# Kernel optimization log

Measured on AMD Instinct MI355X. Metric: run time of the kernel, lower is better.

Reference implementation:

```python
import jax, jax.numpy as jnp
import numpy as np

B, NP, D, K, H = 2, 512, 768, 64, 8
HD = D // H  # head dim = 96


def layernorm(x, g, b, eps=1e-5):
    m = jnp.mean(x, axis=-1, keepdims=True)
    v = jnp.mean((x - m) ** 2, axis=-1, keepdims=True)
    return (x - m) / jnp.sqrt(v + eps) * g + b


def setup_inputs() -> dict:
    key = jax.random.key(0)
    ks = jax.random.split(key, 16)
    s = 0.02
    return {
        "features": jax.random.normal(ks[0], (B, NP, D), jnp.float32),
        "points_xyz": jax.random.normal(ks[1], (B, NP, 3), jnp.float32),
        # distance_encoder: Linear(1 -> D)
        "Wd": jax.random.normal(ks[2], (D,), jnp.float32) * s,
        "bd": jnp.zeros((D,), jnp.float32),
        # geo_attention: MultiheadAttention(D, H)
        "Wq": jax.random.normal(ks[3], (D, D), jnp.float32) * s,
        "bq": jnp.zeros((D,), jnp.float32),
        "Wk": jax.random.normal(ks[4], (D, D), jnp.float32) * s,
        "bk": jnp.zeros((D,), jnp.float32),
        "Wv": jax.random.normal(ks[5], (D, D), jnp.float32) * s,
        "bv": jnp.zeros((D,), jnp.float32),
        "Wo": jax.random.normal(ks[6], (D, D), jnp.float32) * s,
        "bo": jnp.zeros((D,), jnp.float32),
        # spatial_enhancer: Linear(2D -> D) + LayerNorm + SiLU
        "We": jax.random.normal(ks[7], (2 * D, D), jnp.float32) * s,
        "be": jnp.zeros((D,), jnp.float32),
        "g_ln": jnp.ones((D,), jnp.float32),
        "b_ln": jnp.zeros((D,), jnp.float32),
    }


def reference(features, points_xyz, Wd, bd, Wq, bq, Wk, bk, Wv, bv, Wo, bo, We, be, g_ln, b_ln):
    # pairwise distances per batch: [B, Np, Np]
    sq = jnp.sum(points_xyz ** 2, axis=-1)
    d2 = sq[:, :, None] + sq[:, None, :] - 2.0 * jnp.einsum("bnd,bmd->bnm", points_xyz, points_xyz)
    dist = jnp.sqrt(jnp.maximum(d2, 0.0))
    # k nearest neighbors (smallest distances)
    neg_d, idx = jax.lax.top_k(-dist, K)          # idx: [B, Np, K]
    nbr_dist = -neg_d                              # [B, Np, K]
    # gather neighbor features: [B, Np, K, D]
    nbr_feat = jax.vmap(lambda f, i: f[i])(features, idx)
    # distance encoder: Linear(1->D) on unsqueezed distances
    dist_feat = nbr_dist[..., None] * Wd + bd      # [B, Np, K, D]
    kv = nbr_feat + dist_feat
    # multi-head attention: per-point query over its K neighbors
    q = (features @ Wq + bq).reshape(B, NP, H, HD)
    k = (kv @ Wk + bk).reshape(B, NP, K, H, HD)
    v = (kv @ Wv + bv).reshape(B, NP, K, H, HD)
    scores = jnp.einsum("bnhd,bnkhd->bnhk", q, k) / jnp.sqrt(jnp.float32(HD))
    attn = jax.nn.softmax(scores, axis=-1)
    o = jnp.einsum("bnhk,bnkhd->bnhd", attn, v).reshape(B, NP, D)
    attended = o @ Wo + bo                          # [B, Np, D]
    # spatial enhancer on [features ; attended]
    ctx = jnp.concatenate([features, attended], axis=-1)
    enhanced = jax.nn.silu(layernorm(ctx @ We + be, g_ln, b_ln))
    return enhanced
```

## Files before the change

### kernel.cpp

```cpp
#include <hip/hip_runtime.h>
#include <math.h>

#define NPTS 512
#define DIM  768
#define KNN  64
#define NH   8
#define HDIM 96
#define MROWS 1024
#define MPAD  1088
#define WOROWS 832
#define WSQ   ((size_t)DIM * DIM)

typedef unsigned short u16;
typedef unsigned long long ull;
typedef __attribute__((ext_vector_type(8))) short short8;
typedef __attribute__((ext_vector_type(4))) float f32x4;

__device__ __forceinline__ unsigned f2bf(float f) {
    unsigned u = __float_as_uint(f);
    return (u + 0x7fffu + ((u >> 16) & 1u)) >> 16;
}
__device__ __forceinline__ float bf2f(u16 v) {
    return __uint_as_float(((unsigned)v) << 16);
}

__global__ __launch_bounds__(256) void mega_prep_k(
    const float* __restrict__ features,
    const float* __restrict__ Wd, const float* __restrict__ bd,
    const float* __restrict__ Wq, const float* __restrict__ Wk, const float* __restrict__ Wv,
    const float* __restrict__ Wo, const float* __restrict__ bo, const float* __restrict__ We,
    u16* __restrict__ Fb, u16* __restrict__ Wob, u16* __restrict__ W3)
{
    __shared__ float T[64][65];
    int bid = blockIdx.x, tid = threadIdx.x;

    if (bid < 768) {
        int i = (bid * 256 + tid) * 4;
        float4 v = *(const float4*)&features[i];
        uint2 o;
        o.x = f2bf(v.x) | (f2bf(v.y) << 16);
        o.y = f2bf(v.z) | (f2bf(v.w) << 16);
        *(uint2*)&Fb[i] = o;
        return;
    }
    if (bid < 816) {
        int flat = (bid - 768) * 1024 + tid * 4;
        int r = flat / DIM, c = flat - r * DIM;
        uint2 o; o.x = 0u; o.y = 0u;
        if (r == 0) {
            float4 v = *(const float4*)&Wd[c];
            o.x = f2bf(v.x) | (f2bf(v.y) << 16);
            o.y = f2bf(v.z) | (f2bf(v.w) << 16);
        } else if (r == 1) {
            float4 v = *(const float4*)&bd[c];
            o.x = f2bf(v.x) | (f2bf(v.y) << 16);
            o.y = f2bf(v.z) | (f2bf(v.w) << 16);
        }
        *(uint2*)&Fb[(size_t)(MROWS + r) * DIM + c] = o;
        return;
    }
    if (bid < 1440) {
        int flat = (bid - 816) * 1024 + tid * 4;
        int r = flat / DIM, c = flat - r * DIM;
        uint2 o; o.x = 0u; o.y = 0u;
        if (r < DIM) {
            float4 v = *(const float4*)&Wo[(size_t)r * DIM + c];
            o.x = f2bf(v.x) | (f2bf(v.y) << 16);
            o.y = f2bf(v.z) | (f2bf(v.w) << 16);
        } else if (r == DIM) {
            float4 v = *(const float4*)&bo[c];
            o.x = f2bf(v.x) | (f2bf(v.y) << 16);
            o.y = f2bf(v.z) | (f2bf(v.w) << 16);
        }
        *(uint2*)&Wob[(size_t)r * DIM + c] = o;
        return;
    }
    {
        int t = bid - 1440;
        int m = t / 144, r2 = t % 144;
        int by = r2 / 12, bx = r2 % 12;
        const float* S = (m == 0) ? Wq : (m == 1) ? Wk : (m == 2) ? Wv
                       : (m == 3) ? We : (We + WSQ);
        u16* D = W3 + (size_t)m * WSQ;
        int r0 = by * 64, c0 = bx * 64;
#pragma unroll
        for (int i = 0; i < 16; ++i) {
            int lin = tid + i * 256;
            int r = lin >> 6, c = lin & 63;
            T[r][c] = S[(size_t)(r0 + r) * DIM + c0 + c];
        }
        __syncthreads();
#pragma unroll
        for (int i = 0; i < 16; ++i) {
            int lin = tid + i * 256;
            int c = lin >> 6, r = lin & 63;
            D[(size_t)(c0 + c) * DIM + r0 + r] = (u16)f2bf(T[r][c]);
        }
    }
}

union alignas(16) GTSm {
    struct { short As[64][72]; short Bs[64][72]; } g;
    float P[NPTS * 3];
};

__global__ __launch_bounds__(256) void qkvw_topk_k(
    const u16* __restrict__ Fb, const u16* __restrict__ Wob, const u16* __restrict__ W3,
    const float* __restrict__ bq, const float* __restrict__ be,
    const float* __restrict__ pts,
    float* __restrict__ FQ, u16* __restrict__ FKb, u16* __restrict__ FVb,
    u16* __restrict__ WeffT, float* __restrict__ c_e, float* __restrict__ Z0,
    int* __restrict__ idxb, float* __restrict__ distb)
{
    __shared__ GTSm sm;
    int bid = blockIdx.x, tid = threadIdx.x;

    if (bid < 256) {
        int w = tid >> 6, lane = tid & 63;
        int bn = bid * 4 + w;
        int b  = bn >> 9;
        int n  = bn & (NPTS - 1);
        const float* pb = pts + (size_t)b * NPTS * 3;
        for (int i = tid; i < NPTS * 3; i += 256) sm.P[i] = pb[i];
        __syncthreads();

        float xn = sm.P[n * 3], yn = sm.P[n * 3 + 1], zn = sm.P[n * 3 + 2];
        float sqn = xn * xn + yn * yn + zn * zn;
        ull key[8];
#pragma unroll
        for (int r = 0; r < 8; ++r) {
            int m = r * 64 + lane;
            float xm = sm.P[m * 3], ym = sm.P[m * 3 + 1], zm = sm.P[m * 3 + 2];
            float d2 = sqn + (xm * xm + ym * ym + zm * zm)
                     - 2.0f * (xn * xm + yn * ym + zn * zm);
            unsigned db = __float_as_uint(fmaxf(d2, 0.0f));
            key[r] = ((ull)db << 32) | (unsigned)m;
        }

#pragma unroll
        for (int k = 2; k <= 512; k <<= 1) {
#pragma unroll
            for (int j = k >> 1; j > 0; j >>= 1) {
                if (j >= 64) {
                    int jr = j >> 6;
#pragma unroll
                    for (int r = 0; r < 8; ++r) {
                        if ((r & jr) == 0) {
                            int rp = r | jr;
                            bool up = (((r << 6) & k) == 0);
                            ull a = key[r], bk = key[rp];
                            bool alt = a < bk;
                            ull lo = alt ? a : bk, hi = alt ? bk : a;
                            key[r]  = up ? lo : hi;
                            key[rp] = up ? hi : lo;
                        }
                    }
                } else {
#pragma unroll
                    for (int r = 0; r < 8; ++r) {
                        unsigned lo32 = (unsigned)key[r];
                        unsigned hi32 = (unsigned)(key[r] >> 32);
                        unsigned plo = __shfl_xor(lo32, j);
                        unsigned phi = __shfl_xor(hi32, j);
                        ull p = ((ull)phi << 32) | plo;
                        bool keep_lo = ((((r << 6) | lane) & k) == 0) == ((lane & j) == 0);
                        bool alt = key[r] < p;
                        ull lo = alt ? key[r] : p, hi = alt ? p : key[r];
                        key[r] = keep_lo ? lo : hi;
                    }
                }
            }
        }

        ull k0 = key[0];
        idxb[(size_t)bn * KNN + lane]  = (int)(k0 & 0xffffffffu);
        distb[(size_t)bn * KNN + lane] = sqrtf(__uint_as_float((unsigned)(k0 >> 32)));
        return;
    }

    int bid2 = bid - 256;
    int z, by, bx;
    if (bid2 < 816) {
        z = bid2 / 204;
        int rem = bid2 - z * 204;
        by = rem / 12; bx = rem - by * 12;
        if (z == 0 && by >= 16) return;
        if (z == 3 && by >= 13) return;
    } else {
        z = 4;
        int rem = bid2 - 816;
        by = rem / 12; bx = rem - by * 12;
    }
    const u16* A  = (z == 3) ? Wob : Fb;
    const u16* BT = W3 + (size_t)((z == 3) ? 4 : (z == 4) ? 3 : z) * WSQ;

    int wave = tid >> 6, lane = tid & 63;
    int wr = (wave >> 1) * 32, wc = (wave & 1) * 32;
    int l15 = lane & 15, kg = lane >> 4;
    int brow = by * 64, bcol = bx * 64;

    f32x4 acc[2][2] = {};

    int srow = tid >> 3;
    int scol = (tid & 7) * 8;

    for (int k0 = 0; k0 < DIM; k0 += 64) {
#pragma unroll
        for (int s = 0; s < 2; ++s) {
            int r = srow + s * 32;
            *(short8*)&sm.g.As[r][scol] = *(const short8*)&A[(size_t)(brow + r) * DIM + k0 + scol];
            *(short8*)&sm.g.Bs[r][scol] = *(const short8*)&BT[(size_t)(bcol + r) * DIM + k0 + scol];
        }
        __syncthreads();
#pragma unroll
        for (int kk = 0; kk < 2; ++kk) {
            short8 a0 = *(const short8*)&sm.g.As[wr + l15][kk * 32 + kg * 8];
            short8 a1 = *(const short8*)&sm.g.As[wr + 16 + l15][kk * 32 + kg * 8];
            short8 b0 = *(const short8*)&sm.g.Bs[wc + l15][kk * 32 + kg * 8];
            short8 b1 = *(const short8*)&sm.g.Bs[wc + 16 + l15][kk * 32 + kg * 8];
            acc[0][0] = __builtin_amdgcn_mfma_f32_16x16x32_bf16(a0, b0, acc[0][0], 0, 0, 0);
            acc[0][1] = __builtin_amdgcn_mfma_f32_16x16x32_bf16(a0, b1, acc[0][1], 0, 0, 0);
            acc[1][0] = __builtin_amdgcn_mfma_f32_16x16x32_bf16(a1, b0, acc[1][0], 0, 0, 0);
            acc[1][1] = __builtin_amdgcn_mfma_f32_16x16x32_bf16(a1, b1, acc[1][1], 0, 0, 0);
        }
        __syncthreads();
    }

#pragma unroll
    for (int m = 0; m < 2; ++m) {
#pragma unroll
        for (int n = 0; n < 2; ++n) {
            int col  = bcol + wc + n * 16 + l15;
            int row0 = brow + wr + m * 16 + kg * 4;
            if (z == 0) {
                float bv = bq[col];
#pragma unroll
                for (int j = 0; j < 4; ++j)
                    FQ[(size_t)(row0 + j) * DIM + col] = acc[m][n][j] + bv;
            } else if (z == 1) {
#pragma unroll
                for (int j = 0; j < 4; ++j)
                    FKb[(size_t)(row0 + j) * DIM + col] = (u16)f2bf(acc[m][n][j]);
            } else if (z == 2) {
#pragma unroll
                for (int j = 0; j < 4; ++j)
                    FVb[(size_t)(row0 + j) * DIM + col] = (u16)f2bf(acc[m][n][j]);
            } else if (z == 4) {
                float bv = be[col];
#pragma unroll
                for (int j = 0; j < 4; ++j)
                    Z0[(size_t)(row0 + j) * DIM + col] = acc[m][n][j] + bv;
            } else {
                if (row0 + 3 < DIM) {
                    ull pk =
                          (ull)f2bf(acc[m][n][0])
                        | ((ull)f2bf(acc[m][n][1]) << 16)
                        | ((ull)f2bf(acc[m][n][2]) << 32)
                        | ((ull)f2bf(acc[m][n][3]) << 48);
                    *(ull*)&WeffT[(size_t)col * DIM + row0] = pk;
                } else {
#pragma unroll
                    for (int j = 0; j < 4; ++j) {
                        int row = row0 + j;
                        if (row < DIM)       WeffT[(size_t)col * DIM + row] = (u16)f2bf(acc[m][n][j]);
                        else if (row == DIM) c_e[col] = acc[m][n][j];
                    }
                }
            }
        }
    }
}

__global__ __launch_bounds__(256) void gemm_z1_k(
    const u16* __restrict__ Ob, const u16* __restrict__ WeffT,
    const float* __restrict__ c_e, float* __restrict__ Z1)
{
    __shared__ short As[64][72];
    __shared__ short Bs[64][72];

    int tid  = threadIdx.x;
    int wave = tid >> 6, lane = tid & 63;
    int wr = (wave >> 1) * 32, wc = (wave & 1) * 32;
    int l15 = lane & 15, kg = lane >> 4;
    int brow = blockIdx.y * 64, bcol = blockIdx.x * 64;

    f32x4 acc[2][2] = {};

    int srow = tid >> 3;
    int scol = (tid & 7) * 8;

    for (int k0 = 0; k0 < DIM; k0 += 64) {
#pragma unroll
        for (int s = 0; s < 2; ++s) {
            int r = srow + s * 32;
            *(short8*)&As[r][scol] = *(const short8*)&Ob[(size_t)(brow + r) * DIM + k0 + scol];
            *(short8*)&Bs[r][scol] = *(const short8*)&WeffT[(size_t)(bcol + r) * DIM + k0 + scol];
        }
        __syncthreads();
#pragma unroll
        for (int kk = 0; kk < 2; ++kk) {
            short8 a0 = *(const short8*)&As[wr + l15][kk * 32 + kg * 8];
            short8 a1 = *(const short8*)&As[wr + 16 + l15][kk * 32 + kg * 8];
            short8 b0 = *(const short8*)&Bs[wc + l15][kk * 32 + kg * 8];
            short8 b1 = *(const short8*)&Bs[wc + 16 + l15][kk * 32 + kg * 8];
            acc[0][0] = __builtin_amdgcn_mfma_f32_16x16x32_bf16(a0, b0, acc[0][0], 0, 0, 0);
            acc[0][1] = __builtin_amdgcn_mfma_f32_16x16x32_bf16(a0, b1, acc[0][1], 0, 0, 0);
            acc[1][0] = __builtin_amdgcn_mfma_f32_16x16x32_bf16(a1, b0, acc[1][0], 0, 0, 0);
            acc[1][1] = __builtin_amdgcn_mfma_f32_16x16x32_bf16(a1, b1, acc[1][1], 0, 0, 0);
        }
        __syncthreads();
    }

#pragma unroll
    for (int m = 0; m < 2; ++m) {
#pragma unroll
        for (int n = 0; n < 2; ++n) {
            int col = bcol + wc + n * 16 + l15;
            float bv = c_e[col];
#pragma unroll
            for (int j = 0; j < 4; ++j) {
                int row = brow + wr + m * 16 + kg * 4 + j;
                Z1[(size_t)row * DIM + col] = acc[m][n][j] + bv;
            }
        }
    }
}

__global__ __launch_bounds__(512) void attn_k(
    const float* __restrict__ FQ, const u16* __restrict__ FKb, const u16* __restrict__ FVb,
    const int* __restrict__ idxb, const float* __restrict__ distb,
    const float* __restrict__ bk, const float* __restrict__ bv,
    u16* __restrict__ O)
{
    int bn = blockIdx.x;
    int b  = bn >> 9;
    int tid = threadIdx.x;
    int wv = tid >> 6, lane = tid & 63;

    __shared__ float qlds[NH][104];
    __shared__ int   s_idx[KNN];
    __shared__ float s_dist[KNN];
    __shared__ float s_sc[NH][68];
    __shared__ float s_att[NH][68];
    __shared__ float s_qh[NH][2];
    __shared__ float s_sd[NH];

    if (tid < KNN) {
        s_idx[tid]  = idxb[(size_t)bn * KNN + tid];
        s_dist[tid] = distb[(size_t)bn * KNN + tid];
    }
    const float* qrow = FQ + (size_t)bn * DIM;
    {
        int d = tid;
        if (d < DIM) qlds[d / HDIM][d % HDIM] = qrow[d];
        int d2 = tid + 512;
        if (d2 < DIM) qlds[d2 / HDIM][d2 % HDIM] = qrow[d2];
    }
    __syncthreads();

    {
        int h = wv;
        const u16* wdk = FKb + (size_t)MROWS * DIM + h * HDIM;
        const u16* ckr = FKb + (size_t)(MROWS + 1) * DIM + h * HDIM;
        const float* bkh = bk + h * HDIM;
        float q = qlds[h][lane];
        float pw = q * bf2f(wdk[lane]);
        float pc = q * (bf2f(ckr[lane]) + bkh[lane]);
        if (lane < HDIM - 64) {
            float q2 = qlds[h][lane + 64];
            pw = fmaf(q2, bf2f(wdk[lane + 64]), pw);
            pc = fmaf(q2, bf2f(ckr[lane + 64]) + bkh[lane + 64], pc);
        }
#pragma unroll
        for (int off = 32; off; off >>= 1) {
            pw += __shfl_xor(pw, off);
            pc += __shfl_xor(pc, off);
        }
        if (lane == 0) { s_qh[h][0] = pw; s_qh[h][1] = pc; }
    }

    {
        int j = tid >> 3, h = tid & 7;
        const u16* kr = FKb + (size_t)(b * NPTS + s_idx[j]) * DIM + h * HDIM;
        const uint4* kr4 = (const uint4*)kr;
        float a0 = 0.f, a1 = 0.f, a2 = 0.f, a3 = 0.f;
#pragma unroll
        for (int i = 0; i < 12; ++i) {
            uint4 kv = kr4[i];
            float4 qa = *(const float4*)&qlds[h][i * 8];
            float4 qb = *(const float4*)&qlds[h][i * 8 + 4];
            a0 = fmaf(qa.x, __uint_as_float(kv.x << 16), a0);
            a1 = fmaf(qa.y, __uint_as_float(kv.x & 0xffff0000u), a1);
            a2 = fmaf(qa.z, __uint_as_float(kv.y << 16), a2);
            a3 = fmaf(qa.w, __uint_as_float(kv.y & 0xffff0000u), a3);
            a0 = fmaf(qb.x, __uint_as_float(kv.z << 16), a0);
            a1 = fmaf(qb.y, __uint_as_float(kv.z & 0xffff0000u), a1);
            a2 = fmaf(qb.z, __uint_as_float(kv.w << 16), a2);
            a3 = fmaf(qb.w, __uint_as_float(kv.w & 0xffff0000u), a3);
        }
        s_sc[h][j] = (a0 + a1) + (a2 + a3);
    }
    __syncthreads();

    {
        int h = wv, j = lane;
        const float invs = 0.10206207261596575f;
        float qwdk = s_qh[h][0], qck = s_qh[h][1];
        float dj = s_dist[j];
        float sc = (s_sc[h][j] + dj * qwdk + qck) * invs;
        float mx = sc;
#pragma unroll
        for (int off = 32; off; off >>= 1) mx = fmaxf(mx, __shfl_xor(mx, off));
        float ev = __expf(sc - mx);
        float sum = ev;
#pragma unroll
        for (int off = 32; off; off >>= 1) sum += __shfl_xor(sum, off);
        float att = ev / sum;
        s_att[h][j] = att;
        float sd = att * dj;
#pragma unroll
        for (int off = 32; off; off >>= 1) sd += __shfl_xor(sd, off);
        if (lane == 0) s_sd[h] = sd;
    }
    __syncthreads();

    if (tid < 384) {
        int d0 = tid * 2;
        int h  = d0 / HDIM;
        const float* attp = s_att[h];
        const size_t basev = (size_t)(b * NPTS) * DIM + d0;
        float o0 = 0.f, o1 = 0.f;
#pragma unroll 4
        for (int j = 0; j < KNN; ++j) {
            unsigned pv = *(const unsigned*)&FVb[basev + (size_t)s_idx[j] * DIM];
            float a = attp[j];
            o0 = fmaf(a, __uint_as_float(pv << 16), o0);
            o1 = fmaf(a, __uint_as_float(pv & 0xffff0000u), o1);
        }
        const u16* wdv = FVb + (size_t)MROWS * DIM;
        const u16* cvr = FVb + (size_t)(MROWS + 1) * DIM;
        float sdh = s_sd[h];
        o0 += sdh * bf2f(wdv[d0])     + (bf2f(cvr[d0])     + bv[d0]);
        o1 += sdh * bf2f(wdv[d0 + 1]) + (bf2f(cvr[d0 + 1]) + bv[d0 + 1]);
        unsigned po = f2bf(o0) | (f2bf(o1) << 16);
        *(unsigned*)&O[(size_t)bn * DIM + d0] = po;
    }
}

__global__ __launch_bounds__(192) void ln_silu_k(
    const float* __restrict__ Z0, const float* __restrict__ Z1,
    const float* __restrict__ g, const float* __restrict__ bta,
    float* __restrict__ out)
{
    int bn = blockIdx.x, tid = threadIdx.x;
    size_t ro = (size_t)bn * DIM;
    int e0 = tid * 4;
    float4 x = *(const float4*)&Z0[ro + e0];
    {
        float4 p = *(const float4*)&Z1[ro + e0];
        x.x += p.x; x.y += p.y; x.z += p.z; x.w += p.w;
    }
    float s  = (x.x + x.y) + (x.z + x.w);
    float ss = (x.x * x.x + x.y * x.y) + (x.z * x.z + x.w * x.w);
    __shared__ float red[3][2];
#pragma unroll
    for (int off = 32; off; off >>= 1) {
        s  += __shfl_xor(s, off);
        ss += __shfl_xor(ss, off);
    }
    int w = tid >> 6;
    if ((tid & 63) == 0) { red[w][0] = s; red[w][1] = ss; }
    __syncthreads();
    s  = red[0][0] + red[1][0] + red[2][0];
    ss = red[0][1] + red[1][1] + red[2][1];
    float mean = s * (1.0f / DIM);
    float var  = ss * (1.0f / DIM) - mean * mean;
    float rstd = rsqrtf(var + 1e-5f);
    float4 gv = *(const float4*)&g[e0];
    float4 bv = *(const float4*)&bta[e0];
    float4 y;
    y.x = (x.x - mean) * rstd * gv.x + bv.x;
    y.y = (x.y - mean) * rstd * gv.y + bv.y;
    y.z = (x.z - mean) * rstd * gv.z + bv.z;
    y.w = (x.w - mean) * rstd * gv.w + bv.w;
    float4 o;
    o.x = y.x / (1.0f + __expf(-y.x));
    o.y = y.y / (1.0f + __expf(-y.y));
    o.z = y.z / (1.0f + __expf(-y.z));
    o.w = y.w / (1.0f + __expf(-y.w));
    *(float4*)&out[ro + e0] = o;
}

extern "C" void kernel_launch(void* const* d_in, const int* in_sizes, int n_in,
                              void* d_out, int out_size, void* d_ws, size_t ws_size,
                              hipStream_t stream)
{
    const float* features = (const float*)d_in[0];
    const float* pts      = (const float*)d_in[1];
    const float* Wd       = (const float*)d_in[2];
    const float* bd       = (const float*)d_in[3];
    const float* Wq       = (const float*)d_in[4];
    const float* bq       = (const float*)d_in[5];
    const float* Wk       = (const float*)d_in[6];
    const float* bk       = (const float*)d_in[7];
    const float* Wv       = (const float*)d_in[8];
    const float* bv       = (const float*)d_in[9];
    const float* Wo       = (const float*)d_in[10];
    const float* bo       = (const float*)d_in[11];
    const float* We       = (const float*)d_in[12];
    const float* be       = (const float*)d_in[13];
    const float* g_ln     = (const float*)d_in[14];
    const float* b_ln     = (const float*)d_in[15];

    const size_t MAT  = (size_t)MROWS * DIM;
    const size_t MATP = (size_t)MPAD  * DIM;

    float* ws = (float*)d_ws;
    float* FQ    = ws;
    u16*   FKb   = (u16*)(ws + MATP);
    u16*   FVb   = FKb + MATP;
    u16*   Fb    = FVb + MATP;
    u16*   Ob    = Fb + MATP;
    u16*   Wob   = Ob + MAT;
    u16*   W3    = Wob + (size_t)WOROWS * DIM;
    u16*   WeffT = W3 + 5 * WSQ;
    float* c_e   = (float*)(WeffT + WSQ);
    int*   idxb  = (int*)(c_e + DIM);
    float* distb = (float*)(idxb + (size_t)MROWS * KNN);
    float* Z0    = distb + (size_t)MROWS * KNN;
    float* Z1    = Z0 + MAT;

    mega_prep_k<<<2160, 256, 0, stream>>>(features, Wd, bd, Wq, Wk, Wv, Wo, bo, We,
                                          Fb, Wob, W3);
    qkvw_topk_k<<<1264, 256, 0, stream>>>(
        Fb, Wob, W3, bq, be, pts, FQ, FKb, FVb, WeffT, c_e, Z0, idxb, distb);
    attn_k<<<MROWS, 512, 0, stream>>>(FQ, FKb, FVb, idxb, distb, bk, bv, Ob);
    gemm_z1_k<<<dim3(12, 16), 256, 0, stream>>>(Ob, WeffT, c_e, Z1);
    ln_silu_k<<<MROWS, 192, 0, stream>>>(Z0, Z1, g_ln, b_ln, (float*)d_out);
}
```

Measured before the change: 71.68 us.

## Use 128x128 GEMM tiles with direct global-to-LDS loads and XOR swizzle

Both bf16 GEMM paths (the fused QKV/weight-fold kernel and the Z1 GEMM) move from 64x64 to 128x128 block tiles, with each wave computing a 64x64 sub-tile of 4x4 MFMAs. Operand tiles are loaded with global_load_lds straight into shared memory, using an XOR-swizzled column layout in place of padded rows to avoid bank conflicts. Padding of the bf16 buffers is enlarged so the taller tiles stay in bounds. Block counts drop a lot (e.g. 48 blocks for the Z1 GEMM), which raises per-block reuse but lowers occupancy and parallelism on a GPU with many CUs.

New measurement: 77.17 us. +7.7%, slower.

```diff
diff --git a/kernel.cpp b/kernel.cpp
--- a/kernel.cpp
+++ b/kernel.cpp
@@ -7,8 +7,8 @@
 #define NH   8
 #define HDIM 96
 #define MROWS 1024
-#define MPAD  1088
-#define WOROWS 832
+#define MP2   1152
+#define WOR2  896
 #define WSQ   ((size_t)DIM * DIM)
 
 typedef unsigned short u16;
@@ -22,6 +22,11 @@
 }
 __device__ __forceinline__ float bf2f(u16 v) {
     return __uint_as_float(((unsigned)v) << 16);
+}
+__device__ __forceinline__ void gload_lds16(const void* g, void* l) {
+    __builtin_amdgcn_global_load_lds(
+        (const __attribute__((address_space(1))) void*)g,
+        (__attribute__((address_space(3))) void*)l, 16, 0, 0);
 }
 
 __global__ __launch_bounds__(256) void mega_prep_k(
@@ -43,7 +48,7 @@
         *(uint2*)&Fb[i] = o;
         return;
     }
-    if (bid < 816) {
+    if (bid < 864) {
         int flat = (bid - 768) * 1024 + tid * 4;
         int r = flat / DIM, c = flat - r * DIM;
         uint2 o; o.x = 0u; o.y = 0u;
@@ -59,8 +64,8 @@
         *(uint2*)&Fb[(size_t)(MROWS + r) * DIM + c] = o;
         return;
     }
-    if (bid < 1440) {
-        int flat = (bid - 816) * 1024 + tid * 4;
+    if (bid < 1536) {
+        int flat = (bid - 864) * 1024 + tid * 4;
         int r = flat / DIM, c = flat - r * DIM;
         uint2 o; o.x = 0u; o.y = 0u;
         if (r < DIM) {
@@ -76,7 +81,7 @@
         return;
     }
     {
-        int t = bid - 1440;
+        int t = bid - 1536;
         int m = t / 144, r2 = t % 144;
         int by = r2 / 12, bx = r2 % 12;
         const float* S = (m == 0) ? Wq : (m == 1) ? Wk : (m == 2) ? Wv
@@ -100,7 +105,7 @@
 }
 
 union alignas(16) GTSm {
-    struct { short As[64][72]; short Bs[64][72]; } g;
+    struct { short A[128 * 64]; short B[128 * 64]; } g;
     float P[NPTS * 3];
 };
 
@@ -114,10 +119,10 @@
 {
     __shared__ GTSm sm;
     int bid = blockIdx.x, tid = threadIdx.x;
+    int wv = tid >> 6, lane = tid & 63;
 
     if (bid < 256) {
-        int w = tid >> 6, lane = tid & 63;
-        int bn = bid * 4 + w;
+        int bn = bid * 4 + wv;
         int b  = bn >> 9;
         int n  = bn & (NPTS - 1);
         const float* pb = pts + (size_t)b * NPTS * 3;
@@ -180,58 +185,60 @@
 
     int bid2 = bid - 256;
     int z, by, bx;
-    if (bid2 < 816) {
-        z = bid2 / 204;
-        int rem = bid2 - z * 204;
-        by = rem / 12; bx = rem - by * 12;
-        if (z == 0 && by >= 16) return;
-        if (z == 3 && by >= 13) return;
-    } else {
-        z = 4;
-        int rem = bid2 - 816;
-        by = rem / 12; bx = rem - by * 12;
-    }
+    if (bid2 < 162)      { z = bid2 / 54; int r = bid2 % 54; by = r / 6; bx = r % 6; }
+    else if (bid2 < 204) { z = 3; int r = bid2 - 162; by = r / 6; bx = r % 6; }
+    else                 { z = 4; int r = bid2 - 204; by = r / 6; bx = r % 6; }
     const u16* A  = (z == 3) ? Wob : Fb;
     const u16* BT = W3 + (size_t)((z == 3) ? 4 : (z == 4) ? 3 : z) * WSQ;
 
-    int wave = tid >> 6, lane = tid & 63;
-    int wr = (wave >> 1) * 32, wc = (wave & 1) * 32;
+    int wr2 = (wv >> 1) * 64, wc2 = (wv & 1) * 64;
     int l15 = lane & 15, kg = lane >> 4;
-    int brow = by * 64, bcol = bx * 64;
-
-    f32x4 acc[2][2] = {};
-
-    int srow = tid >> 3;
-    int scol = (tid & 7) * 8;
+    int brow = by * 128, bcol = bx * 128;
+
+    f32x4 acc[4][4] = {};
 
     for (int k0 = 0; k0 < DIM; k0 += 64) {
 #pragma unroll
-        for (int s = 0; s < 2; ++s) {
-            int r = srow + s * 32;
-            *(short8*)&sm.g.As[r][scol] = *(const short8*)&A[(size_t)(brow + r) * DIM + k0 + scol];
-            *(short8*)&sm.g.Bs[r][scol] = *(const short8*)&BT[(size_t)(bcol + r) * DIM + k0 + scol];
+        for (int i = 0; i < 4; ++i) {
+            int flat = i * 256 + tid;
+            int row = flat >> 3, c = flat & 7;
+            int cs = c ^ (row & 7);
+            gload_lds16(&A[(size_t)(brow + row) * DIM + k0 + cs * 8],
+                        &sm.g.A[(i * 256 + wv * 64) * 8]);
+            gload_lds16(&BT[(size_t)(bcol + row) * DIM + k0 + cs * 8],
+                        &sm.g.B[(i * 256 + wv * 64) * 8]);
         }
         __syncthreads();
 #pragma unroll
         for (int kk = 0; kk < 2; ++kk) {
-            short8 a0 = *(const short8*)&sm.g.As[wr + l15][kk * 32 + kg * 8];
-            short8 a1 = *(const short8*)&sm.g.As[wr + 16 + l15][kk * 32 + kg * 8];
-            short8 b0 = *(const short8*)&sm.g.Bs[wc + l15][kk * 32 + kg * 8];
-            short8 b1 = *(const short8*)&sm.g.Bs[wc + 16 + l15][kk * 32 + kg * 8];
-            acc[0][0] = __builtin_amdgcn_mfma_f32_16x16x32_bf16(a0, b0, acc[0][0], 0, 0, 0);
-            acc[0][1] = __builtin_amdgcn_mfma_f32_16x16x32_bf16(a0, b1, acc[0][1], 0, 0, 0);
-            acc[1][0] = __builtin_amdgcn_mfma_f32_16x16x32_bf16(a1, b0, acc[1][0], 0, 0, 0);
-            acc[1][1] = __builtin_amdgcn_mfma_f32_16x16x32_bf16(a1, b1, acc[1][1], 0, 0, 0);
+            short8 a[4], b[4];
+#pragma unroll
+            for (int m = 0; m < 4; ++m) {
+                int row = wr2 + m * 16 + l15;
+                int ch = (kk * 4 + kg) ^ (row & 7);
+                a[m] = *(const short8*)&sm.g.A[row * 64 + ch * 8];
+            }
+#pragma unroll
+            for (int n = 0; n < 4; ++n) {
+                int row = wc2 + n * 16 + l15;
+                int ch = (kk * 4 + kg) ^ (row & 7);
+                b[n] = *(const short8*)&sm.g.B[row * 64 + ch * 8];
+            }
+#pragma unroll
+            for (int m = 0; m < 4; ++m)
+#pragma unroll
+                for (int n = 0; n < 4; ++n)
+                    acc[m][n] = __builtin_amdgcn_mfma_f32_16x16x32_bf16(a[m], b[n], acc[m][n], 0, 0, 0);
         }
         __syncthreads();
     }
 
 #pragma unroll
-    for (int m = 0; m < 2; ++m) {
-#pragma unroll
-        for (int n = 0; n < 2; ++n) {
-            int col  = bcol + wc + n * 16 + l15;
-            int row0 = brow + wr + m * 16 + kg * 4;
+    for (int m = 0; m < 4; ++m) {
+#pragma unroll
+        for (int n = 0; n < 4; ++n) {
+            int col  = bcol + wc2 + n * 16 + l15;
+            int row0 = brow + wr2 + m * 16 + kg * 4;
             if (z == 0) {
                 float bv = bq[col];
 #pragma unroll
@@ -275,51 +282,63 @@
     const u16* __restrict__ Ob, const u16* __restrict__ WeffT,
     const float* __restrict__ c_e, float* __restrict__ Z1)
 {
-    __shared__ short As[64][72];
-    __shared__ short Bs[64][72];
-
-    int tid  = threadIdx.x;
-    int wave = tid >> 6, lane = tid & 63;
-    int wr = (wave >> 1) * 32, wc = (wave & 1) * 32;
+    __shared__ short Al[128 * 64];
+    __shared__ short Bl[128 * 64];
+
+    int tid = threadIdx.x;
+    int wv = tid >> 6, lane = tid & 63;
+    int wr2 = (wv >> 1) * 64, wc2 = (wv & 1) * 64;
     int l15 = lane & 15, kg = lane >> 4;
-    int brow = blockIdx.y * 64, bcol = blockIdx.x * 64;
-
-    f32x4 acc[2][2] = {};
-
-    int srow = tid >> 3;
-    int scol = (tid & 7) * 8;
+    int by = blockIdx.x / 6, bx = blockIdx.x % 6;
+    int brow = by * 128, bcol = bx * 128;
+
+    f32x4 acc[4][4] = {};
 
     for (int k0 = 0; k0 < DIM; k0 += 64) {
 #pragma unroll
-        for (int s = 0; s < 2; ++s) {
-            int r = srow + s * 32;
-            *(short8*)&As[r][scol] = *(const short8*)&Ob[(size_t)(brow + r) * DIM + k0 + scol];
-            *(short8*)&Bs[r][scol] = *(const short8*)&WeffT[(size_t)(bcol + r) * DIM + k0 + scol];
+        for (int i = 0; i < 4; ++i) {
+            int flat = i * 256 + tid;
+            int row = flat >> 3, c = flat & 7;
+            int cs = c ^ (row & 7);
+            gload_lds16(&Ob[(size_t)(brow + row) * DIM + k0 + cs * 8],
+                        &Al[(i * 256 + wv * 64) * 8]);
+            gload_lds16(&WeffT[(size_t)(bcol + row) * DIM + k0 + cs * 8],
+                        &Bl[(i * 256 + wv * 64) * 8]);
         }
         __syncthreads();
 #pragma unroll
         for (int kk = 0; kk < 2; ++kk) {
-            short8 a0 = *(const short8*)&As[wr + l15][kk * 32 + kg * 8];
-            short8 a1 = *(const short8*)&As[wr + 16 + l15][kk * 32 + kg * 8];
-            short8 b0 = *(const short8*)&Bs[wc + l15][kk * 32 + kg * 8];
-            short8 b1 = *(const short8*)&Bs[wc + 16 + l15][kk * 32 + kg * 8];
-            acc[0][0] = __builtin_amdgcn_mfma_f32_16x16x32_bf16(a0, b0, acc[0][0], 0, 0, 0);
-            acc[0][1] = __builtin_amdgcn_mfma_f32_16x16x32_bf16(a0, b1, acc[0][1], 0, 0, 0);
-            acc[1][0] = __builtin_amdgcn_mfma_f32_16x16x32_bf16(a1, b0, acc[1][0], 0, 0, 0);
-            acc[1][1] = __builtin_amdgcn_mfma_f32_16x16x32_bf16(a1, b1, acc[1][1], 0, 0, 0);
+            short8 a[4], b[4];
+#pragma unroll
+            for (int m = 0; m < 4; ++m) {
+                int row = wr2 + m * 16 + l15;
+                int ch = (kk * 4 + kg) ^ (row & 7);
+                a[m] = *(const short8*)&Al[row * 64 + ch * 8];
+            }
+#pragma unroll
+            for (int n = 0; n < 4; ++n) {
+                int row = wc2 + n * 16 + l15;
+                int ch = (kk * 4 + kg) ^ (row & 7);
+                b[n] = *(const short8*)&Bl[row * 64 + ch * 8];
+            }
+#pragma unroll
+            for (int m = 0; m < 4; ++m)
+#pragma unroll
+                for (int n = 0; n < 4; ++n)
+                    acc[m][n] = __builtin_amdgcn_mfma_f32_16x16x32_bf16(a[m], b[n], acc[m][n], 0, 0, 0);
         }
         __syncthreads();
     }
 
 #pragma unroll
-    for (int m = 0; m < 2; ++m) {
-#pragma unroll
-        for (int n = 0; n < 2; ++n) {
-            int col = bcol + wc + n * 16 + l15;
+    for (int m = 0; m < 4; ++m) {
+#pragma unroll
+        for (int n = 0; n < 4; ++n) {
+            int col = bcol + wc2 + n * 16 + l15;
             float bv = c_e[col];
 #pragma unroll
             for (int j = 0; j < 4; ++j) {
-                int row = brow + wr + m * 16 + kg * 4 + j;
+                int row = brow + wr2 + m * 16 + kg * 4 + j;
                 Z1[(size_t)row * DIM + col] = acc[m][n][j] + bv;
             }
         }
@@ -513,7 +532,7 @@
     const float* b_ln     = (const float*)d_in[15];
 
     const size_t MAT  = (size_t)MROWS * DIM;
-    const size_t MATP = (size_t)MPAD  * DIM;
+    const size_t MATP = (size_t)MP2 * DIM;
 
     float* ws = (float*)d_ws;
     float* FQ    = ws;
@@ -522,7 +541,7 @@
     u16*   Fb    = FVb + MATP;
     u16*   Ob    = Fb + MATP;
     u16*   Wob   = Ob + MAT;
-    u16*   W3    = Wob + (size_t)WOROWS * DIM;
+    u16*   W3    = Wob + (size_t)WOR2 * DIM;
     u16*   WeffT = W3 + 5 * WSQ;
     float* c_e   = (float*)(WeffT + WSQ);
     int*   idxb  = (int*)(c_e + DIM);
@@ -530,11 +549,11 @@
     float* Z0    = distb + (size_t)MROWS * KNN;
     float* Z1    = Z0 + MAT;
 
-    mega_prep_k<<<2160, 256, 0, stream>>>(features, Wd, bd, Wq, Wk, Wv, Wo, bo, We,
+    mega_prep_k<<<2256, 256, 0, stream>>>(features, Wd, bd, Wq, Wk, Wv, Wo, bo, We,
                                           Fb, Wob, W3);
-    qkvw_topk_k<<<1264, 256, 0, stream>>>(
+    qkvw_topk_k<<<508, 256, 0, stream>>>(
         Fb, Wob, W3, bq, be, pts, FQ, FKb, FVb, WeffT, c_e, Z0, idxb, distb);
     attn_k<<<MROWS, 512, 0, stream>>>(FQ, FKb, FVb, idxb, distb, bk, bv, Ob);
-    gemm_z1_k<<<dim3(12, 16), 256, 0, stream>>>(Ob, WeffT, c_e, Z1);
+    gemm_z1_k<<<48, 256, 0, stream>>>(Ob, WeffT, c_e, Z1);
     ln_silu_k<<<MROWS, 192, 0, stream>>>(Z0, Z1, g_ln, b_ln, (float*)d_out);
 }
```

## Replace full 512-key bitonic sort with sorted-64 chunks and merge-discard top-k

Applied to the files above, without the earlier changes.

The KNN selection no longer sorts all 512 distance keys per point with a full bitonic network. It now sorts eight 64-element chunks in registers, then merges pairs by reversing one sorted chunk, keeping the element-wise minimum, and re-sorting with a half-cleaner. This is done in a tree down to a single list of the 64 smallest. The aim is to cut the compare-exchange and cross-lane shuffle count. It depends on the final merge giving correctly ordered output without the last clean step, which holds only if the output order need not be sorted.

Result: no change. 71.28 us (-0.6%).

```diff
diff --git a/kernel.cpp b/kernel.cpp
--- a/kernel.cpp
+++ b/kernel.cpp
@@ -22,6 +22,26 @@
 }
 __device__ __forceinline__ float bf2f(u16 v) {
     return __uint_as_float(((unsigned)v) << 16);
+}
+__device__ __forceinline__ ull shfl_xor_u64(ull x, int j) {
+    unsigned lo = (unsigned)x, hi = (unsigned)(x >> 32);
+    lo = __shfl_xor(lo, j); hi = __shfl_xor(hi, j);
+    return ((ull)hi << 32) | lo;
+}
+__device__ __forceinline__ ull merge_discard(ull a, ull b, int lane, bool clean) {
+    ull rev = shfl_xor_u64(b, 63);
+    ull m = a < rev ? a : rev;
+    if (clean) {
+#pragma unroll
+        for (int j = 32; j > 0; j >>= 1) {
+            ull p = shfl_xor_u64(m, j);
+            bool keep_lo = ((lane & j) == 0);
+            bool alt = m < p;
+            ull lo = alt ? m : p, hi = alt ? p : m;
+            m = keep_lo ? lo : hi;
+        }
+    }
+    return m;
 }
 
 __global__ __launch_bounds__(256) void mega_prep_k(
@@ -138,39 +158,28 @@
         }
 
 #pragma unroll
-        for (int k = 2; k <= 512; k <<= 1) {
+        for (int k = 2; k <= 64; k <<= 1) {
 #pragma unroll
             for (int j = k >> 1; j > 0; j >>= 1) {
-                if (j >= 64) {
-                    int jr = j >> 6;
-#pragma unroll
-                    for (int r = 0; r < 8; ++r) {
-                        if ((r & jr) == 0) {
-                            int rp = r | jr;
-                            bool up = (((r << 6) & k) == 0);
-                            ull a = key[r], bk = key[rp];
-                            bool alt = a < bk;
-                            ull lo = alt ? a : bk, hi = alt ? bk : a;
-                            key[r]  = up ? lo : hi;
-                            key[rp] = up ? hi : lo;
-                        }
-                    }
-                } else {
-#pragma unroll
-                    for (int r = 0; r < 8; ++r) {
-                        unsigned lo32 = (unsigned)key[r];
-                        unsigned hi32 = (unsigned)(key[r] >> 32);
-                        unsigned plo = __shfl_xor(lo32, j);
-                        unsigned phi = __shfl_xor(hi32, j);
-                        ull p = ((ull)phi << 32) | plo;
-                        bool keep_lo = ((((r << 6) | lane) & k) == 0) == ((lane & j) == 0);
-                        bool alt = key[r] < p;
-                        ull lo = alt ? key[r] : p, hi = alt ? p : key[r];
-                        key[r] = keep_lo ? lo : hi;
-                    }
+#pragma unroll
+                for (int r = 0; r < 8; ++r) {
+                    ull p = shfl_xor_u64(key[r], j);
+                    bool up = ((lane & k) == 0);
+                    bool keep_lo = up == ((lane & j) == 0);
+                    bool alt = key[r] < p;
+                    ull lo = alt ? key[r] : p, hi = alt ? p : key[r];
+                    key[r] = keep_lo ? lo : hi;
                 }
             }
         }
+
+        key[0] = merge_discard(key[0], key[4], lane, true);
+        key[1] = merge_discard(key[1], key[5], lane, true);
+        key[2] = merge_discard(key[2], key[6], lane, true);
+        key[3] = merge_discard(key[3], key[7], lane, true);
+        key[0] = merge_discard(key[0], key[2], lane, true);
+        key[1] = merge_discard(key[1], key[3], lane, true);
+        key[0] = merge_discard(key[0], key[1], lane, false);
 
         ull k0 = key[0];
         idxb[(size_t)bn * KNN + lane]  = (int)(k0 & 0xffffffffu);
```
